# Kernel tuning notes

Measured on AMD Instinct MI355X. Metric: run time of the kernel, lower is better.

## Reference

```python
import jax, jax.numpy as jnp
import numpy as np

N_NODES = 4096
N_EDGES = 131072
D_EDGE = 128
N_HEADS = 8


def setup_inputs() -> dict:
    key = jax.random.key(0)
    k1, k2, k3, k4 = jax.random.split(key, 4)
    edge_index = jax.random.randint(k1, (2, N_EDGES), 0, N_NODES, dtype=jnp.int32)
    edge_attr = jax.random.normal(k2, (N_EDGES, D_EDGE), dtype=jnp.float32)
    W = jax.random.normal(k3, (D_EDGE, N_HEADS), dtype=jnp.float32) * (1.0 / np.sqrt(D_EDGE))
    b = jax.random.normal(k4, (N_HEADS,), dtype=jnp.float32) * 0.01
    return {"edge_index": edge_index, "edge_attr": edge_attr, "W": W, "b": b,
            "num_nodes": N_NODES}


def reference(edge_index, edge_attr, W, b, num_nodes):
    # Linear edge projection: [E, D_edge] @ [D_edge, H] + [H] -> [E, H]
    scores = edge_attr @ W + b
    u = edge_index[0]
    v = edge_index[1]
    H = W.shape[1]
    # Dense bias [H, N, N]; non-edge positions stay 0.
    bias = jnp.zeros((H, num_nodes, num_nodes), dtype=scores.dtype)
    bias = bias.at[:, u, v].set(scores.T)
    return bias
```

## Files before the change

kernel.cpp:

```cpp
#include <hip/hip_runtime.h>

#define N_NODES 4096
#define N_EDGES 131072
#define D_EDGE  128
#define N_HEADS 8

__global__ void edgebias_winner(const int* __restrict__ edge_index,
                                int* __restrict__ out_plane0) {
    int e = blockIdx.x * blockDim.x + threadIdx.x;
    if (e >= N_EDGES) return;
    int u = edge_index[e];
    int v = edge_index[N_EDGES + e];
    atomicMax(&out_plane0[(size_t)u * N_NODES + v], e + 1);
}

__global__ void edgebias_scatter(const int* __restrict__ edge_index,
                                 const float* __restrict__ edge_attr,
                                 const float* __restrict__ W,
                                 const float* __restrict__ b,
                                 float* __restrict__ out) {
    __shared__ float Ws[D_EDGE * N_HEADS];
    __shared__ float bs[N_HEADS];
    for (int i = threadIdx.x; i < D_EDGE * N_HEADS; i += blockDim.x)
        Ws[i] = W[i];
    if (threadIdx.x < N_HEADS) bs[threadIdx.x] = b[threadIdx.x];
    __syncthreads();

    int e = blockIdx.x * blockDim.x + threadIdx.x;
    if (e >= N_EDGES) return;
    int u = edge_index[e];
    int v = edge_index[N_EDGES + e];
    size_t cell = (size_t)u * N_NODES + v;

    const int* out_i = (const int*)out;
    if (out_i[cell] != e + 1) return;

    float acc[N_HEADS];
    #pragma unroll
    for (int h = 0; h < N_HEADS; ++h) acc[h] = bs[h];

    const float4* row = (const float4*)(edge_attr + (size_t)e * D_EDGE);
    #pragma unroll 8
    for (int j = 0; j < D_EDGE / 4; ++j) {
        float4 a = row[j];
        int d = j * 4;
        #pragma unroll
        for (int h = 0; h < N_HEADS; ++h) {
            acc[h] += a.x * Ws[(d + 0) * N_HEADS + h]
                    + a.y * Ws[(d + 1) * N_HEADS + h]
                    + a.z * Ws[(d + 2) * N_HEADS + h]
                    + a.w * Ws[(d + 3) * N_HEADS + h];
        }
    }

    #pragma unroll
    for (int h = 0; h < N_HEADS; ++h)
        out[(size_t)h * N_NODES * N_NODES + cell] = acc[h];
}

extern "C" void kernel_launch(void* const* d_in, const int* in_sizes, int n_in,
                              void* d_out, int out_size, void* d_ws, size_t ws_size,
                              hipStream_t stream) {
    const int*   edge_index = (const int*)  d_in[0];
    const float* edge_attr  = (const float*)d_in[1];
    const float* W          = (const float*)d_in[2];
    const float* b          = (const float*)d_in[3];
    float* out = (float*)d_out;

    size_t out_bytes = (size_t)N_HEADS * N_NODES * N_NODES * sizeof(float);
    hipMemsetAsync(d_out, 0, out_bytes, stream);

    dim3 blk(256);
    dim3 grd((N_EDGES + 255) / 256);
    edgebias_winner<<<grd, blk, 0, stream>>>(edge_index, (int*)d_out);

    edgebias_scatter<<<grd, blk, 0, stream>>>(edge_index, edge_attr, W, b, out);
}
```

Measured before the change: 637.2 us.

## Fuse score projection with winner election and scatter per edge-head thread

Computes all edge scores unconditionally in one kernel that also performs the atomicMax winner election into a separate workspace array, writing scores compactly. A second kernel uses one thread per (edge, head) to check the winner and scatter the score. This is meant to spread the 8 strided output writes over more threads for better memory parallelism. In exchange it adds a 64MB memset of the winner array and computes projections for losing edges too.

```diff
diff --git a/kernel.cpp b/kernel.cpp
--- a/kernel.cpp
+++ b/kernel.cpp
@@ -5,20 +5,15 @@
 #define D_EDGE  128
 #define N_HEADS 8
 
-__global__ void edgebias_winner(const int* __restrict__ edge_index,
-                                int* __restrict__ out_plane0) {
-    int e = blockIdx.x * blockDim.x + threadIdx.x;
-    if (e >= N_EDGES) return;
-    int u = edge_index[e];
-    int v = edge_index[N_EDGES + e];
-    atomicMax(&out_plane0[(size_t)u * N_NODES + v], e + 1);
-}
+#define WS_SCORES_OFF  0
+#define WS_WINNER_OFF  ((size_t)N_EDGES * N_HEADS * sizeof(float))
 
-__global__ void edgebias_scatter(const int* __restrict__ edge_index,
-                                 const float* __restrict__ edge_attr,
-                                 const float* __restrict__ W,
-                                 const float* __restrict__ b,
-                                 float* __restrict__ out) {
+__global__ void edgebias_scores_winner(const int* __restrict__ edge_index,
+                                       const float* __restrict__ edge_attr,
+                                       const float* __restrict__ W,
+                                       const float* __restrict__ b,
+                                       float* __restrict__ scores,
+                                       int* __restrict__ winner) {
     __shared__ float Ws[D_EDGE * N_HEADS];
     __shared__ float bs[N_HEADS];
     for (int i = threadIdx.x; i < D_EDGE * N_HEADS; i += blockDim.x)
@@ -28,12 +23,6 @@
 
     int e = blockIdx.x * blockDim.x + threadIdx.x;
     if (e >= N_EDGES) return;
-    int u = edge_index[e];
-    int v = edge_index[N_EDGES + e];
-    size_t cell = (size_t)u * N_NODES + v;
-
-    const int* out_i = (const int*)out;
-    if (out_i[cell] != e + 1) return;
 
     float acc[N_HEADS];
     #pragma unroll
@@ -53,9 +42,28 @@
         }
     }
 
-    #pragma unroll
-    for (int h = 0; h < N_HEADS; ++h)
-        out[(size_t)h * N_NODES * N_NODES + cell] = acc[h];
+    float4 s0 = make_float4(acc[0], acc[1], acc[2], acc[3]);
+    float4 s1 = make_float4(acc[4], acc[5], acc[6], acc[7]);
+    ((float4*)scores)[(size_t)e * 2 + 0] = s0;
+    ((float4*)scores)[(size_t)e * 2 + 1] = s1;
+
+    int u = edge_index[e];
+    int v = edge_index[N_EDGES + e];
+    atomicMax(&winner[u * N_NODES + v], e + 1);
+}
+
+__global__ void edgebias_scatter(const int* __restrict__ edge_index,
+                                 const float* __restrict__ scores,
+                                 const int* __restrict__ winner,
+                                 float* __restrict__ out) {
+    int t = blockIdx.x * blockDim.x + threadIdx.x;
+    int e = t >> 3;
+    int h = t & 7;
+    int u = edge_index[e];
+    int v = edge_index[N_EDGES + e];
+    size_t cell = (size_t)u * N_NODES + v;
+    if (winner[cell] == e + 1)
+        out[(size_t)h * N_NODES * N_NODES + cell] = scores[t];
 }
 
 extern "C" void kernel_launch(void* const* d_in, const int* in_sizes, int n_in,
@@ -67,12 +75,15 @@
     const float* b          = (const float*)d_in[3];
     float* out = (float*)d_out;
 
-    size_t out_bytes = (size_t)N_HEADS * N_NODES * N_NODES * sizeof(float);
-    hipMemsetAsync(d_out, 0, out_bytes, stream);
+    float* scores = (float*)((char*)d_ws + WS_SCORES_OFF);
+    int*   winner = (int*)  ((char*)d_ws + WS_WINNER_OFF);
 
-    dim3 blk(256);
-    dim3 grd((N_EDGES + 255) / 256);
-    edgebias_winner<<<grd, blk, 0, stream>>>(edge_index, (int*)d_out);
+    hipMemsetAsync(d_out, 0, (size_t)N_HEADS * N_NODES * N_NODES * sizeof(float), stream);
+    hipMemsetAsync(winner, 0, (size_t)N_NODES * N_NODES * sizeof(int), stream);
 
-    edgebias_scatter<<<grd, blk, 0, stream>>>(edge_index, edge_attr, W, b, out);
+    edgebias_scores_winner<<<dim3((N_EDGES + 255) / 256), dim3(256), 0, stream>>>(
+        edge_index, edge_attr, W, b, scores, winner);
+
+    edgebias_scatter<<<dim3((N_EDGES * N_HEADS) / 256), dim3(256), 0, stream>>>(
+        edge_index, scores, winner, out);
 }
```

Measured after the change: 653.7 us. 2.6% more time.
